# Kernel optimization log

Measured on AMD Instinct MI355X. Metric: run time of the kernel, lower is better.

## Reference

```python
import jax, jax.numpy as jnp
import numpy as np

D_MODEL = 1024

def setup_inputs() -> dict:
    key = jax.random.key(0)
    k1, k2 = jax.random.split(key, 2)
    x = jax.random.normal(k1, (4, 2048, D_MODEL), dtype=jnp.float32)
    W_attn = jax.random.normal(k2, (3 * D_MODEL, D_MODEL), dtype=jnp.float32) * (1.0 / np.sqrt(D_MODEL))
    b_attn = jnp.zeros((3 * D_MODEL,), dtype=jnp.float32)
    return {"x": x, "W_attn": W_attn, "b_attn": b_attn}

def reference(x, W_attn, b_attn):
    B, T, C = x.shape
    # fused QKV projection; torch split order is (k, q, v)
    kqv = x @ W_attn.T + b_attn            # [B, T, 3C]
    k, q, v = jnp.split(kqv, 3, axis=-1)   # each [B, T, C]
    # NOTE: original computes k @ q^T (quirk), scaled by sqrt(d_model)
    scores = jnp.einsum('btc,bsc->bts', k, q) / jnp.sqrt(jnp.asarray(C, x.dtype))
    causal = jnp.tril(jnp.ones((T, T), dtype=bool))
    scores = jnp.where(causal[None, :, :], scores, -jnp.inf)
    attn = jax.nn.softmax(scores, axis=-1)
    return jnp.einsum('bts,bsc->btc', attn, v)
```

## Files before the change

### kernel.cpp

```cpp
#include <hip/hip_runtime.h>

typedef __bf16 bf16x8 __attribute__((ext_vector_type(8)));
typedef float f32x4 __attribute__((ext_vector_type(4)));
typedef float fl4 __attribute__((ext_vector_type(4)));
typedef unsigned short us4 __attribute__((ext_vector_type(4)));
typedef unsigned short us8 __attribute__((ext_vector_type(8)));

__device__ __forceinline__ unsigned short f2bf(float f) {
  unsigned u = __builtin_bit_cast(unsigned, f);
  u += 0x7fffu + ((u >> 16) & 1u);
  return (unsigned short)(u >> 16);
}
__device__ __forceinline__ float bf2f(unsigned short h) {
  unsigned u = ((unsigned)h) << 16;
  return __builtin_bit_cast(float, u);
}

__device__ __forceinline__ void async16(const void* g, void* l) {
  __builtin_amdgcn_global_load_lds(
      (const __attribute__((address_space(1))) unsigned int*)g,
      (__attribute__((address_space(3))) unsigned int*)l, 16, 0, 0);
}

#define BARM() asm volatile("s_barrier" ::: "memory")
#define VMCNT4() asm volatile("s_waitcnt vmcnt(4)" ::: "memory")
#define VMCNT6() asm volatile("s_waitcnt vmcnt(6)" ::: "memory")
#define VMCNT8() asm volatile("s_waitcnt vmcnt(8)" ::: "memory")
#define LGKM0() asm volatile("s_waitcnt lgkmcnt(0)" ::: "memory")
#define LGKM8() asm volatile("s_waitcnt lgkmcnt(8)" ::: "memory")
#define SCHEDB() __builtin_amdgcn_sched_barrier(0)

__global__ __launch_bounds__(256) void cvt_bf16_2(const float* __restrict__ sA,
                                                  unsigned short* __restrict__ dA, int nA,
                                                  const float* __restrict__ sB,
                                                  unsigned short* __restrict__ dB, int nB) {
  int i = blockIdx.x * 256 + threadIdx.x;
  const float* s;
  unsigned short* d;
  if (i < nA) {
    s = sA; d = dA;
  } else {
    i -= nA;
    if (i >= nB) return;
    s = sB; d = dB;
  }
  fl4 f = ((const fl4*)s)[i];
  us4 o;
  o[0] = f2bf(f[0]); o[1] = f2bf(f[1]); o[2] = f2bf(f[2]); o[3] = f2bf(f[3]);
  ((us4*)d)[i] = o;
}

__global__ __launch_bounds__(256) void transpose_v(const unsigned short* __restrict__ kqv,
                                                   unsigned short* __restrict__ vT) {
  int b = blockIdx.z;
  int t0 = blockIdx.x * 64;
  int c0 = blockIdx.y * 64;
  __shared__ unsigned short tile[64][68];
  int tid = threadIdx.x;
#pragma unroll
  for (int i = 0; i < 4; ++i) {
    int idx = i * 256 + tid;
    int r = idx >> 4;
    int c4 = (idx & 15) * 4;
    const unsigned short* src = kqv + ((size_t)(b * 2048 + t0 + r)) * 3072 + 2048 + c0 + c4;
    us4 v = *(const us4*)src;
    *(us4*)&tile[r][c4] = v;
  }
  __syncthreads();
#pragma unroll
  for (int i = 0; i < 4; ++i) {
    int idx = i * 256 + tid;
    int rc = idx >> 4;
    int t4 = (idx & 15) * 4;
    us4 v;
    v[0] = tile[t4 + 0][rc]; v[1] = tile[t4 + 1][rc];
    v[2] = tile[t4 + 2][rc]; v[3] = tile[t4 + 3][rc];
    unsigned short* dst = vT + ((size_t)(b * 1024 + c0 + rc)) * 2048 + t0 + t4;
    *(us4*)dst = v;
  }
}

__global__ __launch_bounds__(512, 2) void gemm_g0(
    const unsigned short* __restrict__ A, const unsigned short* __restrict__ B,
    unsigned short* __restrict__ C, const float* __restrict__ bias) {
  const int flat = blockIdx.x;
  const int swz = (flat & 7) * 64 + (flat >> 3);
  const int bx = swz & 7;
  const int by = swz >> 3;
  const int rowBase = by * 128, colBase = bx * 384;
  const int lda = 1024, ldc = 3072, nk = 16;

  __shared__ __align__(16) unsigned char lds[131072];
  const int tid = threadIdx.x;
  const int lane = tid & 63, wid = tid >> 6;
  const int wr = wid >> 2, wc = wid & 3;
  const int l15 = lane & 15, l4 = lane >> 4, l7 = lane & 7;

  f32x4 acc[4][6] = {};
  bf16x8 af01[2][2], af23[2][2], bf[6][2];

  const unsigned short* Ab = A + (size_t)rowBase * lda;
  const unsigned short* Bb = B + (size_t)colBase * lda;
  unsigned aoff[2], boff[6], aldso[2], bldso[6];
#pragma unroll
  for (int i = 0; i < 6; ++i) {
    int off = i * 8192 + tid * 16;
    int r = off >> 7;
    int sb = ((off >> 4) & 7) ^ (r & 7);
    if (i < 2) { aoff[i] = (unsigned)(r * lda + sb * 8); aldso[i] = (unsigned)off; }
    boff[i] = (unsigned)(r * lda + sb * 8);
    bldso[i] = (unsigned)off;
  }

  auto STA = [&](int bufc, int op, int koff) {
    async16(Ab + (size_t)(aoff[op] + (unsigned)koff), lds + bufc * 65536 + aldso[op]);
  };
  auto STB = [&](int bufc, int op, int koff) {
    async16(Bb + (size_t)(boff[op] + (unsigned)koff),
            lds + bufc * 65536 + 16384 + bldso[op]);
  };
  auto RA = [&](int bufc, int m, int kk) -> bf16x8 {
    int row = wr * 64 + m * 16 + l15;
    int blk = (kk * 4 + l4) ^ l7;
    return *(const bf16x8*)(lds + bufc * 65536 + row * 128 + blk * 16);
  };
  auto RB = [&](int bufc, int n, int kk) -> bf16x8 {
    int row = wc * 96 + n * 16 + l15;
    int blk = (kk * 4 + l4) ^ l7;
    return *(const bf16x8*)(lds + bufc * 65536 + 16384 + row * 128 + blk * 16);
  };

#define RD_A01(BUF)                                                            \
  _Pragma("unroll") for (int mi = 0; mi < 2; ++mi)                             \
  _Pragma("unroll") for (int kk = 0; kk < 2; ++kk) af01[mi][kk] = RA((BUF), mi, kk)
#define RD_A23(BUF)                                                            \
  _Pragma("unroll") for (int mi = 0; mi < 2; ++mi)                             \
  _Pragma("unroll") for (int kk = 0; kk < 2; ++kk) af23[mi][kk] = RA((BUF), 2 + mi, kk)
#define RD_B(BUF, N0)                                                          \
  _Pragma("unroll") for (int nj = 0; nj < 3; ++nj)                             \
  _Pragma("unroll") for (int kk = 0; kk < 2; ++kk) bf[(N0) + nj][kk] = RB((BUF), (N0) + nj, kk)

#define MQ(MB, NB, AF)                                                         \
  _Pragma("unroll") for (int kk = 0; kk < 2; ++kk)                             \
  _Pragma("unroll") for (int mi = 0; mi < 2; ++mi)                             \
  _Pragma("unroll") for (int nj = 0; nj < 3; ++nj)                             \
      acc[(MB) + mi][(NB) + nj] = __builtin_amdgcn_mfma_f32_16x16x32_bf16(     \
          AF[mi][kk], bf[(NB) + nj][kk], acc[(MB) + mi][(NB) + nj], 0, 0, 0)

#define PHASE(RDS, STG, GATE, MB, NB, AF)                                      \
  do {                                                                         \
    RDS;                                                                       \
    STG;                                                                       \
    BARM();                                                                    \
    LGKM0();                                                                   \
    SCHEDB();                                                                  \
    __builtin_amdgcn_s_setprio(1);                                             \
    MQ(MB, NB, AF);                                                            \
    __builtin_amdgcn_s_setprio(0);                                             \
    GATE;                                                                      \
    BARM();                                                                    \
  } while (0)

  STA(0, 0, 0); STA(0, 1, 0);
#pragma unroll
  for (int i = 0; i < 6; ++i) STB(0, i, 0);
#pragma unroll
  for (int i = 0; i < 6; ++i) STB(1, i, 64);
  VMCNT6();
  BARM();

  for (int it = 0; it < 8; ++it) {
    int t = it * 2;
    int kA1 = (t + 1) * 64;
    int k2 = (t + 2 < nk - 1 ? t + 2 : nk - 1) * 64;
    int k3 = (t + 3 < nk - 1 ? t + 3 : nk - 1) * 64;
    PHASE({ RD_A01(0); RD_B(0, 0); }, { STA(1, 0, kA1); STA(1, 1, kA1); },
          (void)0, 0, 0, af01);
    PHASE({ RD_A23(0); RD_B(0, 3); }, (void)0, (void)0, 0, 3, af01);
    PHASE({}, { STB(0, 0, k2); STB(0, 1, k2); STB(0, 2, k2); },
          (void)0, 2, 3, af23);
    PHASE({}, { STB(0, 3, k2); STB(0, 4, k2); STB(0, 5, k2); },
          VMCNT6(), 2, 0, af23);
    PHASE({ RD_A01(1); RD_B(1, 0); }, { STA(0, 0, k2); STA(0, 1, k2); },
          (void)0, 0, 0, af01);
    PHASE({ RD_A23(1); RD_B(1, 3); }, (void)0, (void)0, 0, 3, af01);
    PHASE({}, { STB(1, 0, k3); STB(1, 1, k3); STB(1, 2, k3); },
          (void)0, 2, 3, af23);
    PHASE({}, { STB(1, 3, k3); STB(1, 4, k3); STB(1, 5, k3); },
          VMCNT6(), 2, 0, af23);
  }
#undef PHASE
#undef MQ
#undef RD_A01
#undef RD_A23
#undef RD_B

  const int cr = l4 * 4;
#pragma unroll
  for (int n = 0; n < 6; ++n) {
    int col = colBase + wc * 96 + n * 16 + l15;
    float bv = bias[col];
#pragma unroll
    for (int m = 0; m < 4; ++m) {
      int row = rowBase + wr * 64 + m * 16 + cr;
#pragma unroll
      for (int i = 0; i < 4; ++i)
        C[(size_t)(row + i) * ldc + col] = f2bf(acc[m][n][i] + bv);
    }
  }
}

__global__ __launch_bounds__(512, 2) void gemm_s(
    const unsigned short* __restrict__ A, int lda, long long sA,
    const unsigned short* __restrict__ B, int ldb, long long sB,
    unsigned short* __restrict__ C, int ldc, long long sC,
    float scale, int K) {
  int bx = blockIdx.x, by = blockIdx.y;
  const int bz = blockIdx.z;
  if (bx > by) return;
  A += (size_t)bz * sA;
  B += (size_t)bz * sB;
  const int rowBase = by * 256;
  const int colBase = bx * 256;
  const int nk = K / 64;

  __shared__ __align__(16) unsigned char lds[131072];
  const int tid = threadIdx.x;
  const int lane = tid & 63;
  const int wid = tid >> 6;
  const int wr = wid >> 2;
  const int wc = wid & 3;
  const int l15 = lane & 15, l4 = lane >> 4, l7 = lane & 7;

  f32x4 acc[8][4] = {};
  bf16x8 af0[4][2], af1[4][2], bf0[2][2], bf1[2][2];

  const unsigned short* Ab = A + (size_t)rowBase * lda;
  const unsigned short* Bb = B + (size_t)colBase * ldb;
  unsigned loff[2][2];
  unsigned lldso[2];
#pragma unroll
  for (int i = 0; i < 2; ++i) {
    int off = (i * 512 + tid) * 16;
    int r = off >> 7;
    int sb = ((off >> 4) & 7) ^ (r & 7);
    lldso[i] = (unsigned)off;
#pragma unroll
    for (int hh = 0; hh < 2; ++hh)
      loff[hh][i] = (unsigned)((hh * 128 + r) * lda + sb * 8);
  }

  auto STAGE = [&](int bufc, int isB, int half, const unsigned short* Gb, int koff) {
#pragma unroll
    for (int i = 0; i < 2; ++i)
      async16(Gb + (size_t)(loff[half][i] + (unsigned)koff),
              lds + bufc * 65536 + isB * 32768 + half * 16384 + lldso[i]);
  };
  auto RDA = [&](int bufc, int m, int kk) -> bf16x8 {
    int row = m * 16 + l15;
    int blk = (kk * 4 + l4) ^ l7;
    return *(const bf16x8*)(lds + bufc * 65536 + wr * 16384 + row * 128 + blk * 16);
  };
  auto RDB = [&](int bufc, int n, int kk) -> bf16x8 {
    int row = (wc & 1) * 64 + n * 16 + l15;
    int blk = (kk * 4 + l4) ^ l7;
    return *(const bf16x8*)(lds + bufc * 65536 + 32768 + (wc >> 1) * 16384 +
                            row * 128 + blk * 16);
  };

#define RDA8(dst, BUF, Q)                                                      \
  _Pragma("unroll") for (int mi = 0; mi < 4; ++mi)                             \
  _Pragma("unroll") for (int kk = 0; kk < 2; ++kk)                             \
      dst[mi][kk] = RDA((BUF), (Q) * 4 + mi, kk)
#define RDB4(dst, BUF, NB)                                                     \
  _Pragma("unroll") for (int nj = 0; nj < 2; ++nj)                             \
  _Pragma("unroll") for (int kk = 0; kk < 2; ++kk)                             \
      dst[nj][kk] = RDB((BUF), (NB) + nj, kk)

#define MFMAQ(MB, NB, AF, BF)                                                  \
  _Pragma("unroll") for (int kk = 0; kk < 2; ++kk)                             \
  _Pragma("unroll") for (int mi = 0; mi < 4; ++mi)                             \
  _Pragma("unroll") for (int nj = 0; nj < 2; ++nj)                             \
      acc[(MB) + mi][(NB) + nj] = __builtin_amdgcn_mfma_f32_16x16x32_bf16(     \
          AF[mi][kk], BF[nj][kk], acc[(MB) + mi][(NB) + nj], 0, 0, 0)

#define PH(RDS, STG, HINT, GATE, MB, NB, AF, BF)                               \
  do {                                                                         \
    RDS;                                                                       \
    STG;                                                                       \
    HINT;                                                                      \
    BARM();                                                                    \
    LGKM0();                                                                   \
    SCHEDB();                                                                  \
    __builtin_amdgcn_s_setprio(1);                                             \
    MFMAQ(MB, NB, AF, BF);                                                     \
    __builtin_amdgcn_s_setprio(0);                                             \
    GATE;                                                                      \
    BARM();                                                                    \
  } while (0)

  STAGE(0, 0, 0, Ab, 0);
  STAGE(0, 0, 1, Ab, 0);
  STAGE(0, 1, 0, Bb, 0);
  STAGE(0, 1, 1, Bb, 0);
  STAGE(1, 1, 0, Bb, 64);
  STAGE(1, 1, 1, Bb, 64);
  VMCNT4();
  BARM();

  const int nt2 = nk >> 1;
  for (int it = 0; it < nt2; ++it) {
    int t = it * 2;
    int kA1 = (t + 1) * 64;
    int k2 = (t + 2 < nk - 1 ? t + 2 : nk - 1) * 64;
    int k3 = (t + 3 < nk - 1 ? t + 3 : nk - 1) * 64;
    PH({ RDA8(af0, 0, 0); RDB4(bf0, 0, 0); }, STAGE(1, 0, 0, Ab, kA1), LGKM8(),
       (void)0, 0, 0, af0, bf0);
    PH({ RDB4(bf1, 0, 2); }, STAGE(1, 0, 1, Ab, kA1), (void)0,
       (void)0, 0, 2, af0, bf1);
    PH({ RDA8(af1, 0, 1); }, STAGE(0, 1, 0, Bb, k2), (void)0,
       (void)0, 4, 2, af1, bf1);
    PH({}, STAGE(0, 1, 1, Bb, k2), (void)0,
       VMCNT4(), 4, 0, af1, bf0);
    PH({ RDA8(af0, 1, 0); RDB4(bf0, 1, 0); }, STAGE(0, 0, 0, Ab, k2), LGKM8(),
       (void)0, 0, 0, af0, bf0);
    PH({ RDB4(bf1, 1, 2); }, STAGE(0, 0, 1, Ab, k2), (void)0,
       (void)0, 0, 2, af0, bf1);
    PH({ RDA8(af1, 1, 1); }, STAGE(1, 1, 0, Bb, k3), (void)0,
       (void)0, 4, 2, af1, bf1);
    PH({}, STAGE(1, 1, 1, Bb, k3), (void)0,
       VMCNT4(), 4, 0, af1, bf0);
  }
#undef PH
#undef MFMAQ
#undef RDA8
#undef RDB4

  const int cr = l4 * 4;
  unsigned short* Cb = C + (size_t)bz * sC;
#pragma unroll
  for (int n = 0; n < 4; ++n) {
    int col = colBase + wc * 64 + n * 16 + l15;
#pragma unroll
    for (int m = 0; m < 8; ++m) {
      int row = rowBase + wr * 128 + m * 16 + cr;
#pragma unroll
      for (int i = 0; i < 4; ++i)
        Cb[(size_t)(row + i) * ldc + col] = f2bf(acc[m][n][i] * scale);
    }
  }
}

__global__ __launch_bounds__(256, 2) void gemm_pv2(
    const unsigned short* __restrict__ S, const unsigned short* __restrict__ V,
    float* __restrict__ O) {
  const int f = blockIdx.x;
  const int bx = f & 7;
  const int p = (f >> 3) & 7;
  const int bz = f >> 6;
  const int byH = 15 - p;
  const int nkL = 2 * (p + 1);
  const int nkH = 32 - 2 * p;
  const unsigned short* base = S + (size_t)bz * 2048 * 2048;
  const unsigned short* AH = base + (size_t)(byH * 128) * 2048;
  const unsigned short* AL = base + (size_t)(p * 128) * 2048;
  const unsigned short* Bb = V + (size_t)bz * 1024 * 2048 + (size_t)(bx * 128) * 2048;
  float* Ob = O + (size_t)bz * 2048 * 1024;

  __shared__ __align__(16) unsigned char lds[65536];
  const int tid = threadIdx.x;
  const int lane = tid & 63, wid = tid >> 6;
  const int wr = (wid >> 1) * 64, wc = (wid & 1) * 64;
  const int l15 = lane & 15, l4 = lane >> 4, l7 = lane & 7;

  f32x4 accH[4][4] = {}, accL[4][4] = {};

  unsigned goff[4], ldso[4];
#pragma unroll
  for (int ii = 0; ii < 4; ++ii) {
    int off = (ii * 256 + tid) * 16;
    int rr = off >> 7;
    int sb = ((off >> 4) & 7) ^ (rr & 7);
    goff[ii] = (unsigned)(rr * 2048 + sb * 8);
    ldso[ii] = (unsigned)off;
  }

  auto ST = [&](int buf, const unsigned short* Ap, unsigned kof) {
#pragma unroll
    for (int ii = 0; ii < 4; ++ii) {
      async16(Ap + (size_t)(goff[ii] + kof), lds + buf * 32768 + ldso[ii]);
      async16(Bb + (size_t)(goff[ii] + kof), lds + buf * 32768 + 16384 + ldso[ii]);
    }
  };
  auto ITEM = [&](int i, const unsigned short*& P, unsigned& kf) {
    if (i < 2 * nkL) {
      P = (i & 1) ? AL : AH;
      kf = (unsigned)((i >> 1) * 64);
    } else {
      P = AH;
      kf = (unsigned)((i - nkL) * 64);
    }
  };

#define PVSTEP(BUF, ACC, NITEM)                                                \
  do {                                                                         \
    const unsigned short* nP;                                                  \
    unsigned nK;                                                               \
    ITEM((NITEM) < 33 ? (NITEM) : 33, nP, nK);                                 \
    VMCNT8();                                                                  \
    BARM();                                                                    \
    bf16x8 af[4][2], bfr[4][2];                                                \
    _Pragma("unroll") for (int m = 0; m < 4; ++m) {                            \
      int row = wr + m * 16 + l15;                                             \
      _Pragma("unroll") for (int kk = 0; kk < 2; ++kk)                         \
        af[m][kk] = *(const bf16x8*)(lds + (BUF) * 32768 + row * 128 +         \
                                     (((kk * 4 + l4) ^ l7) * 16));             \
    }                                                                          \
    _Pragma("unroll") for (int n = 0; n < 4; ++n) {                            \
      int row = wc + n * 16 + l15;                                             \
      _Pragma("unroll") for (int kk = 0; kk < 2; ++kk)                         \
        bfr[n][kk] = *(const bf16x8*)(lds + (BUF) * 32768 + 16384 + row * 128 +\
                                      (((kk * 4 + l4) ^ l7) * 16));            \
    }                                                                          \
    LGKM0();                                                                   \
    BARM();                                                                    \
    ST((BUF), nP, nK);                                                         \
    SCHEDB();                                                                  \
    __builtin_amdgcn_s_setprio(1);                                             \
    _Pragma("unroll") for (int kk = 0; kk < 2; ++kk)                           \
    _Pragma("unroll") for (int m = 0; m < 4; ++m)                              \
    _Pragma("unroll") for (int n = 0; n < 4; ++n)                              \
      ACC[m][n] = __builtin_amdgcn_mfma_f32_16x16x32_bf16(af[m][kk], bfr[n][kk],\
                                                          ACC[m][n], 0, 0, 0); \
    __builtin_amdgcn_s_setprio(0);                                             \
  } while (0)

  ST(0, AH, 0);
  {
    const unsigned short* P; unsigned kf;
    ITEM(1, P, kf);
    ST(1, P, kf);
  }

  for (int t = 0; t < nkL; ++t) {
    PVSTEP(0, accH, 2 * t + 2);
    PVSTEP(1, accL, 2 * t + 3);
  }
  for (int u = nkL; u < nkH; u += 2) {
    PVSTEP(0, accH, u + nkL + 2);
    PVSTEP(1, accH, u + nkL + 3);
  }
#undef PVSTEP

  const int cr = l4 * 4;
#pragma unroll
  for (int n = 0; n < 4; ++n) {
    int col = bx * 128 + wc + n * 16 + l15;
#pragma unroll
    for (int m = 0; m < 4; ++m) {
      int rH = byH * 128 + wr + m * 16 + cr;
      int rL = p * 128 + wr + m * 16 + cr;
#pragma unroll
      for (int i = 0; i < 4; ++i) {
        Ob[(size_t)(rH + i) * 1024 + col] = accH[m][n][i];
        Ob[(size_t)(rL + i) * 1024 + col] = accL[m][n][i];
      }
    }
  }
}

__global__ __launch_bounds__(256) void softmax_causal(unsigned short* __restrict__ S) {
  const int T = 2048;
  int t = blockIdx.x, b = blockIdx.y;
  unsigned short* row = S + ((size_t)b * T + t) * T;
  const int nv = t + 1;
  const int bound = ((t >> 7) + 1) << 7;
  int tid = threadIdx.x;
  int lane = tid & 63, wid = tid >> 6;
  int s0 = tid * 8;
  us8 raw = {};
  if (s0 < nv) raw = *(const us8*)(row + s0);
  float v[8];
  float m = -3.0e38f;
#pragma unroll
  for (int j = 0; j < 8; ++j) {
    v[j] = bf2f(raw[j]);
    if (s0 + j < nv) m = fmaxf(m, v[j]);
  }
#pragma unroll
  for (int o = 32; o > 0; o >>= 1) m = fmaxf(m, __shfl_xor(m, o, 64));
  __shared__ float red[4];
  if (lane == 0) red[wid] = m;
  __syncthreads();
  m = fmaxf(fmaxf(red[0], red[1]), fmaxf(red[2], red[3]));
  __syncthreads();
  float sum = 0.f;
#pragma unroll
  for (int j = 0; j < 8; ++j) {
    float e = (s0 + j < nv) ? exp2f(v[j] - m) : 0.f;
    v[j] = e;
    sum += e;
  }
#pragma unroll
  for (int o = 32; o > 0; o >>= 1) sum += __shfl_xor(sum, o, 64);
  if (lane == 0) red[wid] = sum;
  __syncthreads();
  sum = red[0] + red[1] + red[2] + red[3];
  float inv = 1.0f / sum;
  if (s0 < bound) {
    us8 outv;
#pragma unroll
    for (int j = 0; j < 8; ++j) outv[j] = f2bf(v[j] * inv);
    *(us8*)(row + s0) = outv;
  }
}

extern "C" void kernel_launch(void* const* d_in, const int* in_sizes, int n_in,
                              void* d_out, int out_size, void* d_ws, size_t ws_size,
                              hipStream_t stream) {
  const float* x = (const float*)d_in[0];
  const float* W = (const float*)d_in[1];
  const float* bias = (const float*)d_in[2];
  float* out = (float*)d_out;

  char* ws = (char*)d_ws;
  if (ws_size < 106954752u) return;
  unsigned short* xbf = (unsigned short*)(ws);
  unsigned short* vT = xbf;
  unsigned short* wbf = (unsigned short*)(ws + 16777216);
  unsigned short* kqv = (unsigned short*)(ws + 23068672);
  unsigned short* S = (unsigned short*)(ws + 73400320);

  const float kSoftmaxScale = 1.4426950408889634f / 32.0f;

  cvt_bf16_2<<<11264, 256, 0, stream>>>(x, xbf, 2097152, W, wbf, 786432);

  gemm_g0<<<dim3(512, 1, 1), 512, 0, stream>>>(xbf, wbf, kqv, bias);

  transpose_v<<<dim3(32, 16, 4), 256, 0, stream>>>(kqv, vT);

  gemm_s<<<dim3(8, 8, 4), 512, 0, stream>>>(
      kqv, 3072, 2048LL * 3072, kqv + 1024, 3072, 2048LL * 3072,
      S, 2048, 2048LL * 2048, kSoftmaxScale, 1024);

  softmax_causal<<<dim3(2048, 4), 256, 0, stream>>>(S);

  gemm_pv2<<<dim3(256, 1, 1), 256, 0, stream>>>(S, vT, out);
}
```

Before: 167.6 us.

## Enlarge QKV GEMM tile to 256x384 with BK=32 and 256 blocks

The QKV projection GEMM now uses 256-row tiles instead of 128 and halves the K step to 32, with a new 4-block XOR swizzle for 64-byte LDS rows and a rebuilt 8-phase schedule. The grid drops from 512 to 256 blocks and LDS per block shrinks from 128KB to 80KB. The aim is higher arithmetic intensity per block and less global traffic for the shared B tile. In exchange each wave holds twice as many accumulators (192 VGPRs for acc alone), which risks register pressure or spills under launch_bounds(512,2), and with 256 blocks the grid may fill the CUs only once.

```diff
diff --git a/kernel.cpp b/kernel.cpp
--- a/kernel.cpp
+++ b/kernel.cpp
@@ -23,8 +23,8 @@
 }
 
 #define BARM() asm volatile("s_barrier" ::: "memory")
+#define VMCNT3() asm volatile("s_waitcnt vmcnt(3)" ::: "memory")
 #define VMCNT4() asm volatile("s_waitcnt vmcnt(4)" ::: "memory")
-#define VMCNT6() asm volatile("s_waitcnt vmcnt(6)" ::: "memory")
 #define VMCNT8() asm volatile("s_waitcnt vmcnt(8)" ::: "memory")
 #define LGKM0() asm volatile("s_waitcnt lgkmcnt(0)" ::: "memory")
 #define LGKM8() asm volatile("s_waitcnt lgkmcnt(8)" ::: "memory")
@@ -84,68 +84,62 @@
     const unsigned short* __restrict__ A, const unsigned short* __restrict__ B,
     unsigned short* __restrict__ C, const float* __restrict__ bias) {
   const int flat = blockIdx.x;
-  const int swz = (flat & 7) * 64 + (flat >> 3);
-  const int bx = swz & 7;
-  const int by = swz >> 3;
-  const int rowBase = by * 128, colBase = bx * 384;
-  const int lda = 1024, ldc = 3072, nk = 16;
-
-  __shared__ __align__(16) unsigned char lds[131072];
+  const int swz = (flat & 7) * 32 + (flat >> 3);
+  const int bx = swz >> 5;
+  const int by = swz & 31;
+  const int rowBase = by * 256, colBase = bx * 384;
+  const int lda = 1024, ldc = 3072, nk = 32;
+
+  __shared__ __align__(16) unsigned char lds[81920];
   const int tid = threadIdx.x;
   const int lane = tid & 63, wid = tid >> 6;
   const int wr = wid >> 2, wc = wid & 3;
-  const int l15 = lane & 15, l4 = lane >> 4, l7 = lane & 7;
-
-  f32x4 acc[4][6] = {};
-  bf16x8 af01[2][2], af23[2][2], bf[6][2];
+  const int l15 = lane & 15, l4 = lane >> 4;
+
+  f32x4 acc[8][6] = {};
+  bf16x8 af0[4], af1[4], bf[6];
 
   const unsigned short* Ab = A + (size_t)rowBase * lda;
   const unsigned short* Bb = B + (size_t)colBase * lda;
-  unsigned aoff[2], boff[6], aldso[2], bldso[6];
-#pragma unroll
-  for (int i = 0; i < 6; ++i) {
+  unsigned aoff[2], boff[3], aldso[2], bldso[3];
+#pragma unroll
+  for (int i = 0; i < 3; ++i) {
     int off = i * 8192 + tid * 16;
-    int r = off >> 7;
-    int sb = ((off >> 4) & 7) ^ (r & 7);
+    int r = off >> 6;
+    int sb = ((off >> 4) & 3) ^ ((r >> 1) & 3);
     if (i < 2) { aoff[i] = (unsigned)(r * lda + sb * 8); aldso[i] = (unsigned)off; }
     boff[i] = (unsigned)(r * lda + sb * 8);
     bldso[i] = (unsigned)off;
   }
 
-  auto STA = [&](int bufc, int op, int koff) {
-    async16(Ab + (size_t)(aoff[op] + (unsigned)koff), lds + bufc * 65536 + aldso[op]);
-  };
-  auto STB = [&](int bufc, int op, int koff) {
+  auto STA = [&](int buf, int op, int koff) {
+    async16(Ab + (size_t)(aoff[op] + (unsigned)koff), lds + buf * 40960 + aldso[op]);
+  };
+  auto STB = [&](int buf, int op, int koff) {
     async16(Bb + (size_t)(boff[op] + (unsigned)koff),
-            lds + bufc * 65536 + 16384 + bldso[op]);
-  };
-  auto RA = [&](int bufc, int m, int kk) -> bf16x8 {
-    int row = wr * 64 + m * 16 + l15;
-    int blk = (kk * 4 + l4) ^ l7;
-    return *(const bf16x8*)(lds + bufc * 65536 + row * 128 + blk * 16);
-  };
-  auto RB = [&](int bufc, int n, int kk) -> bf16x8 {
+            lds + buf * 40960 + 16384 + bldso[op]);
+  };
+  auto RA = [&](int buf, int m) -> bf16x8 {
+    int row = wr * 128 + m * 16 + l15;
+    return *(const bf16x8*)(lds + buf * 40960 + row * 64 +
+                            (((l4 ^ (row >> 1)) & 3) * 16));
+  };
+  auto RB = [&](int buf, int n) -> bf16x8 {
     int row = wc * 96 + n * 16 + l15;
-    int blk = (kk * 4 + l4) ^ l7;
-    return *(const bf16x8*)(lds + bufc * 65536 + 16384 + row * 128 + blk * 16);
-  };
-
-#define RD_A01(BUF)                                                            \
-  _Pragma("unroll") for (int mi = 0; mi < 2; ++mi)                             \
-  _Pragma("unroll") for (int kk = 0; kk < 2; ++kk) af01[mi][kk] = RA((BUF), mi, kk)
-#define RD_A23(BUF)                                                            \
-  _Pragma("unroll") for (int mi = 0; mi < 2; ++mi)                             \
-  _Pragma("unroll") for (int kk = 0; kk < 2; ++kk) af23[mi][kk] = RA((BUF), 2 + mi, kk)
-#define RD_B(BUF, N0)                                                          \
-  _Pragma("unroll") for (int nj = 0; nj < 3; ++nj)                             \
-  _Pragma("unroll") for (int kk = 0; kk < 2; ++kk) bf[(N0) + nj][kk] = RB((BUF), (N0) + nj, kk)
+    return *(const bf16x8*)(lds + buf * 40960 + 16384 + row * 64 +
+                            (((l4 ^ (row >> 1)) & 3) * 16));
+  };
+
+#define RD_A03(BUF) _Pragma("unroll") for (int mi = 0; mi < 4; ++mi) af0[mi] = RA((BUF), mi)
+#define RD_A47(BUF) _Pragma("unroll") for (int mi = 0; mi < 4; ++mi) af1[mi] = RA((BUF), 4 + mi)
+#define RD_B02(BUF) _Pragma("unroll") for (int nj = 0; nj < 3; ++nj) bf[nj] = RB((BUF), nj)
+#define RD_B35(BUF) _Pragma("unroll") for (int nj = 0; nj < 3; ++nj) bf[3 + nj] = RB((BUF), 3 + nj)
 
 #define MQ(MB, NB, AF)                                                         \
-  _Pragma("unroll") for (int kk = 0; kk < 2; ++kk)                             \
-  _Pragma("unroll") for (int mi = 0; mi < 2; ++mi)                             \
+  _Pragma("unroll") for (int mi = 0; mi < 4; ++mi)                             \
   _Pragma("unroll") for (int nj = 0; nj < 3; ++nj)                             \
       acc[(MB) + mi][(NB) + nj] = __builtin_amdgcn_mfma_f32_16x16x32_bf16(     \
-          AF[mi][kk], bf[(NB) + nj][kk], acc[(MB) + mi][(NB) + nj], 0, 0, 0)
+          AF[mi], bf[(NB) + nj], acc[(MB) + mi][(NB) + nj], 0, 0, 0)
 
 #define PHASE(RDS, STG, GATE, MB, NB, AF)                                      \
   do {                                                                         \
@@ -163,37 +157,36 @@
 
   STA(0, 0, 0); STA(0, 1, 0);
 #pragma unroll
-  for (int i = 0; i < 6; ++i) STB(0, i, 0);
-#pragma unroll
-  for (int i = 0; i < 6; ++i) STB(1, i, 64);
-  VMCNT6();
+  for (int i = 0; i < 3; ++i) STB(0, i, 0);
+#pragma unroll
+  for (int i = 0; i < 3; ++i) STB(1, i, 32);
+  VMCNT3();
   BARM();
 
-  for (int it = 0; it < 8; ++it) {
+  for (int it = 0; it < 16; ++it) {
     int t = it * 2;
-    int kA1 = (t + 1) * 64;
-    int k2 = (t + 2 < nk - 1 ? t + 2 : nk - 1) * 64;
-    int k3 = (t + 3 < nk - 1 ? t + 3 : nk - 1) * 64;
-    PHASE({ RD_A01(0); RD_B(0, 0); }, { STA(1, 0, kA1); STA(1, 1, kA1); },
-          (void)0, 0, 0, af01);
-    PHASE({ RD_A23(0); RD_B(0, 3); }, (void)0, (void)0, 0, 3, af01);
-    PHASE({}, { STB(0, 0, k2); STB(0, 1, k2); STB(0, 2, k2); },
-          (void)0, 2, 3, af23);
-    PHASE({}, { STB(0, 3, k2); STB(0, 4, k2); STB(0, 5, k2); },
-          VMCNT6(), 2, 0, af23);
-    PHASE({ RD_A01(1); RD_B(1, 0); }, { STA(0, 0, k2); STA(0, 1, k2); },
-          (void)0, 0, 0, af01);
-    PHASE({ RD_A23(1); RD_B(1, 3); }, (void)0, (void)0, 0, 3, af01);
-    PHASE({}, { STB(1, 0, k3); STB(1, 1, k3); STB(1, 2, k3); },
-          (void)0, 2, 3, af23);
-    PHASE({}, { STB(1, 3, k3); STB(1, 4, k3); STB(1, 5, k3); },
-          VMCNT6(), 2, 0, af23);
+    int kA1 = (t + 1) * 32;
+    int k2 = (t + 2 < nk - 1 ? t + 2 : nk - 1) * 32;
+    int k3 = (t + 3 < nk - 1 ? t + 3 : nk - 1) * 32;
+    PHASE({ RD_A03(0); RD_B02(0); }, { STA(1, 0, kA1); STA(1, 1, kA1); },
+          (void)0, 0, 0, af0);
+    PHASE({ RD_B35(0); }, (void)0, (void)0, 0, 3, af0);
+    PHASE({ RD_A47(0); }, { STB(0, 0, k2); STB(0, 1, k2); STB(0, 2, k2); },
+          (void)0, 4, 3, af1);
+    PHASE({}, (void)0, VMCNT3(), 4, 0, af1);
+    PHASE({ RD_A03(1); RD_B02(1); }, { STA(0, 0, k2); STA(0, 1, k2); },
+          (void)0, 0, 0, af0);
+    PHASE({ RD_B35(1); }, (void)0, (void)0, 0, 3, af0);
+    PHASE({ RD_A47(1); }, { STB(1, 0, k3); STB(1, 1, k3); STB(1, 2, k3); },
+          (void)0, 4, 3, af1);
+    PHASE({}, (void)0, VMCNT3(), 4, 0, af1);
   }
 #undef PHASE
 #undef MQ
-#undef RD_A01
-#undef RD_A23
-#undef RD_B
+#undef RD_A03
+#undef RD_A47
+#undef RD_B02
+#undef RD_B35
 
   const int cr = l4 * 4;
 #pragma unroll
@@ -201,8 +194,8 @@
     int col = colBase + wc * 96 + n * 16 + l15;
     float bv = bias[col];
 #pragma unroll
-    for (int m = 0; m < 4; ++m) {
-      int row = rowBase + wr * 64 + m * 16 + cr;
+    for (int m = 0; m < 8; ++m) {
+      int row = rowBase + wr * 128 + m * 16 + cr;
 #pragma unroll
       for (int i = 0; i < 4; ++i)
         C[(size_t)(row + i) * ldc + col] = f2bf(acc[m][n][i] + bv);
@@ -535,7 +528,7 @@
 
   cvt_bf16_2<<<11264, 256, 0, stream>>>(x, xbf, 2097152, W, wbf, 786432);
 
-  gemm_g0<<<dim3(512, 1, 1), 512, 0, stream>>>(xbf, wbf, kqv, bias);
+  gemm_g0<<<dim3(256, 1, 1), 512, 0, stream>>>(xbf, wbf, kqv, bias);
 
   transpose_v<<<dim3(32, 16, 4), 256, 0, stream>>>(kqv, vT);
 
```

After: 177.6 us. 1.06x slower.

## Triple-buffer LDS in PV GEMM to drop the second barrier per step

Applied to the files above, without the earlier changes.

The PV GEMM goes from double-buffered to triple-buffered LDS staging, raising shared memory to 96KB and launch bounds to one block per CU. Each step now issues the next async global-to-LDS load into the third buffer right after the first barrier. That removes the LGKM wait, the second barrier and the scheduling fence that used to protect reuse of the buffer being read. The aim is fewer syncs and more load/compute overlap, at the cost of occupancy and a more complex modulo-3 buffer rotation.

```diff
diff --git a/kernel.cpp b/kernel.cpp
--- a/kernel.cpp
+++ b/kernel.cpp
@@ -351,7 +351,7 @@
   }
 }
 
-__global__ __launch_bounds__(256, 2) void gemm_pv2(
+__global__ __launch_bounds__(256, 1) void gemm_pv3(
     const unsigned short* __restrict__ S, const unsigned short* __restrict__ V,
     float* __restrict__ O) {
   const int f = blockIdx.x;
@@ -367,7 +367,7 @@
   const unsigned short* Bb = V + (size_t)bz * 1024 * 2048 + (size_t)(bx * 128) * 2048;
   float* Ob = O + (size_t)bz * 2048 * 1024;
 
-  __shared__ __align__(16) unsigned char lds[65536];
+  __shared__ __align__(16) unsigned char lds[98304];
   const int tid = threadIdx.x;
   const int lane = tid & 63, wid = tid >> 6;
   const int wr = (wid >> 1) * 64, wc = (wid & 1) * 64;
@@ -409,6 +409,7 @@
     ITEM((NITEM) < 33 ? (NITEM) : 33, nP, nK);                                 \
     VMCNT8();                                                                  \
     BARM();                                                                    \
+    ST(((NITEM) % 3), nP, nK);                                                 \
     bf16x8 af[4][2], bfr[4][2];                                                \
     _Pragma("unroll") for (int m = 0; m < 4; ++m) {                            \
       int row = wr + m * 16 + l15;                                             \
@@ -422,10 +423,6 @@
         bfr[n][kk] = *(const bf16x8*)(lds + (BUF) * 32768 + 16384 + row * 128 +\
                                       (((kk * 4 + l4) ^ l7) * 16));            \
     }                                                                          \
-    LGKM0();                                                                   \
-    BARM();                                                                    \
-    ST((BUF), nP, nK);                                                         \
-    SCHEDB();                                                                  \
     __builtin_amdgcn_s_setprio(1);                                             \
     _Pragma("unroll") for (int kk = 0; kk < 2; ++kk)                           \
     _Pragma("unroll") for (int m = 0; m < 4; ++m)                              \
@@ -442,13 +439,22 @@
     ST(1, P, kf);
   }
 
-  for (int t = 0; t < nkL; ++t) {
-    PVSTEP(0, accH, 2 * t + 2);
-    PVSTEP(1, accL, 2 * t + 3);
-  }
-  for (int u = nkL; u < nkH; u += 2) {
-    PVSTEP(0, accH, u + nkL + 2);
-    PVSTEP(1, accH, u + nkL + 3);
+  {
+    int s = 0;
+    for (; s < 2 * nkL; s += 2) {
+      switch (s % 3) {
+        case 0: PVSTEP(0, accH, s + 2); PVSTEP(1, accL, s + 3); break;
+        case 1: PVSTEP(1, accH, s + 2); PVSTEP(2, accL, s + 3); break;
+        default: PVSTEP(2, accH, s + 2); PVSTEP(0, accL, s + 3); break;
+      }
+    }
+    for (; s < 34; s += 2) {
+      switch (s % 3) {
+        case 0: PVSTEP(0, accH, s + 2); PVSTEP(1, accH, s + 3); break;
+        case 1: PVSTEP(1, accH, s + 2); PVSTEP(2, accH, s + 3); break;
+        default: PVSTEP(2, accH, s + 2); PVSTEP(0, accH, s + 3); break;
+      }
+    }
   }
 #undef PVSTEP
 
@@ -545,5 +551,5 @@
 
   softmax_causal<<<dim3(2048, 4), 256, 0, stream>>>(S);
 
-  gemm_pv2<<<dim3(256, 1, 1), 256, 0, stream>>>(S, vT, out);
-}
+  gemm_pv3<<<dim3(256, 1, 1), 256, 0, stream>>>(S, vT, out);
+}
```

After: 169.1 us. Within noise of the previous version (+0.9%).
